# Kernel tuning notes

Hardware: AMD Instinct MI355X
Metric: run time of the kernel (lower is better)

## Reference

```python
import jax, jax.numpy as jnp
import numpy as np

H = 4096          # hidden_size
I = 11008         # intermediate_size
G = 128           # AWQ group_size
# AWQ interleaved nibble order within each packed int32
_ORDER = jnp.array([0, 4, 1, 5, 2, 6, 3, 7], dtype=jnp.int32) * 4


def _mk_lin(key, K, N):
    k1, k2, k3 = jax.random.split(key, 3)
    qw = jax.random.randint(k1, (K, N // 8), 0, 100, dtype=jnp.int32)
    qz = jax.random.randint(k2, (K // G, N // 8), 0, 100, dtype=jnp.int32)
    sc = jax.random.normal(k3, (K // G, N), dtype=jnp.float32) * 0.02
    return qw, qz, sc


def setup_inputs() -> dict:
    key = jax.random.key(0)
    ks = jax.random.split(key, 7)
    x = jax.random.normal(ks[0], (8, 16, H), dtype=jnp.float32)
    ln1_w = jnp.ones((H,), dtype=jnp.float32)
    ln2_w = jnp.ones((H,), dtype=jnp.float32)
    qkv_qw, qkv_qz, qkv_sc = _mk_lin(ks[1], H, 3 * H)
    o_qw, o_qz, o_sc = _mk_lin(ks[2], H, H)
    gu_qw, gu_qz, gu_sc = _mk_lin(ks[3], H, 2 * I)
    dn_qw, dn_qz, dn_sc = _mk_lin(ks[4], I, H)
    return dict(x=x, ln1_w=ln1_w, ln2_w=ln2_w,
                qkv_qw=qkv_qw, qkv_qz=qkv_qz, qkv_sc=qkv_sc,
                o_qw=o_qw, o_qz=o_qz, o_sc=o_sc,
                gu_qw=gu_qw, gu_qz=gu_qz, gu_sc=gu_sc,
                dn_qw=dn_qw, dn_qz=dn_qz, dn_sc=dn_sc)


def rmsnorm(x, w, eps=1e-6):
    return x * jax.lax.rsqrt(jnp.mean(x * x, axis=-1, keepdims=True) + eps) * w


def dequant(qw, qz, sc):
    # qw: [K, N//8] int32 -> [K, N]; qz: [K//G, N//8] -> [K//G, N]
    K = qw.shape[0]
    N = sc.shape[1]
    w = ((qw[:, :, None] >> _ORDER) & 0xF).reshape(K, N).astype(sc.dtype)
    z = ((qz[:, :, None] >> _ORDER) & 0xF).reshape(K // G, N).astype(sc.dtype)
    return (w - jnp.repeat(z, G, axis=0)) * jnp.repeat(sc, G, axis=0)


def lite_linear(x, qw, qz, sc):
    return x @ dequant(qw, qz, sc)


def reference(x, ln1_w, ln2_w,
              qkv_qw, qkv_qz, qkv_sc,
              o_qw, o_qz, o_sc,
              gu_qw, gu_qz, gu_sc,
              dn_qw, dn_qz, dn_sc):
    residual = x
    h = rmsnorm(x, ln1_w)
    h = lite_linear(h, qkv_qw, qkv_qz, qkv_sc)[..., :H]  # mock attn: take q slice
    h = lite_linear(h, o_qw, o_qz, o_sc)
    h = residual + h
    residual = h
    h = rmsnorm(h, ln2_w)
    gate_up = lite_linear(h, gu_qw, gu_qz, gu_sc)
    gate, up = gate_up[..., :I], gate_up[..., I:]
    h = lite_linear(jax.nn.silu(gate) * up, dn_qw, dn_qz, dn_sc)
    return residual + h
```

## Files before the change

kernel.cpp:

```cpp
#include <hip/hip_runtime.h>

typedef unsigned int   u32;
typedef unsigned short u16;

typedef __bf16 bf16x8 __attribute__((ext_vector_type(8)));
typedef float  f32x4  __attribute__((ext_vector_type(4)));

#define M_TOK 128

__device__ __forceinline__ u16 f2bf(float f) {
    u32 u = __builtin_bit_cast(u32, f);
    return (u16)((u + 0x8000u) >> 16);
}
__device__ __forceinline__ float bf2f(u16 h) {
    u32 u = ((u32)h) << 16;
    return __builtin_bit_cast(float, u);
}

__device__ __forceinline__ int rowoff(int r) { return r * 80 + (r >> 3) * 64; }

__launch_bounds__(256)
__global__ void rmsnorm_k(const float* __restrict__ in, const float* __restrict__ w,
                          u16* __restrict__ out) {
    const int row = blockIdx.x;
    const float* x = in + (size_t)row * 4096;
    float ss = 0.f;
#pragma unroll
    for (int j = 0; j < 16; ++j) {
        float v = x[threadIdx.x + 256 * j];
        ss += v * v;
    }
#pragma unroll
    for (int off = 32; off > 0; off >>= 1) ss += __shfl_down(ss, off, 64);
    __shared__ float ws4[4];
    if ((threadIdx.x & 63) == 0) ws4[threadIdx.x >> 6] = ss;
    __syncthreads();
    float total = ws4[0] + ws4[1] + ws4[2] + ws4[3];
    float r = rsqrtf(total * (1.f / 4096.f) + 1e-6f);
    u16* o = out + (size_t)row * 4096;
#pragma unroll
    for (int j = 0; j < 16; ++j) {
        int i = threadIdx.x + 256 * j;
        o[i] = f2bf(x[i] * r * w[i]);
    }
}

__launch_bounds__(256, 3)
__global__ void gemm_awq(const u16* __restrict__ A, const int* __restrict__ qw,
                         const int* __restrict__ qz, const float* __restrict__ sc,
                         u16* __restrict__ part,
                         int Astride, int qws, int scs, int N, int K, int kchunk) {
    __shared__ __align__(16) char ldsA[11264];
    __shared__ __align__(16) char ldsB[5632];

    const int tid = threadIdx.x;
    const int n0 = blockIdx.x * 64;
    const int sk = blockIdx.y;
    const int kc0 = sk * kchunk;
    const int kend = min(kc0 + kchunk, K);

    const int w    = tid >> 6;
    const int lane = tid & 63;
    const int wr  = (w >> 1) * 64;
    const int wc  = (w & 1) * 32;
    const int q   = lane >> 4;
    const int l16 = lane & 15;

    const int kp = tid & 15;
    const int p  = (tid >> 4) & 7;
    const int pc = (n0 >> 3) + p;
    const int nb = p * 704;

    const int ar = tid & 127;
    const u16* arow = A + (size_t)ar * Astride;
    char* adst = ldsA + rowoff(ar);

    f32x4 acc[4][2] = {};
    const u32 M4 = 0x0F0F0F0Fu;

    u32 zv = 0, w0c = 0, w1c = 0;
    float scv[8];
    uint4 a0c, a1c, a2c, a3c;
    if (tid < 128) {
        zv  = (u32)qz[(size_t)(kc0 >> 7) * qws + pc];
        const float* scp = sc + (size_t)(kc0 >> 7) * scs + n0 + p * 8;
        *(float4*)&scv[0] = *(const float4*)&scp[0];
        *(float4*)&scv[4] = *(const float4*)&scp[4];
        w0c = (u32)qw[(size_t)(kc0 + 2 * kp) * qws + pc];
        w1c = (u32)qw[(size_t)(kc0 + 2 * kp + 1) * qws + pc];
    } else {
        a0c = *(const uint4*)&arow[kc0 + 0];
        a1c = *(const uint4*)&arow[kc0 + 8];
        a2c = *(const uint4*)&arow[kc0 + 16];
        a3c = *(const uint4*)&arow[kc0 + 24];
    }

    for (int g0 = kc0; g0 < kend; g0 += 128) {
        const bool moreg = (g0 + 128) < kend;
        u32 zv_n = 0;
        float scv_n[8];
        u32 be = 0, bo = 0;
        if (tid < 128) {
            be = 0x10101010u - (zv & M4);
            bo = 0x10101010u - ((zv >> 4) & M4);
        }
#pragma unroll
        for (int s = 0; s < 4; ++s) {
            const int k0 = g0 + s * 32;
            const int kn = k0 + 32;
            if (tid < 128) {
                const u32 w0 = w0c, w1 = w1c;
                if (kn < kend) {
                    w0c = (u32)qw[(size_t)(kn + 2 * kp) * qws + pc];
                    w1c = (u32)qw[(size_t)(kn + 2 * kp + 1) * qws + pc];
                }
                if (s == 0 && moreg) {
                    zv_n = (u32)qz[(size_t)((g0 + 128) >> 7) * qws + pc];
                    const float* scp = sc + (size_t)((g0 + 128) >> 7) * scs + n0 + p * 8;
                    *(float4*)&scv_n[0] = *(const float4*)&scp[0];
                    *(float4*)&scv_n[4] = *(const float4*)&scp[4];
                }
                const u32 d0e = (w0 & M4) + be;
                const u32 d0o = ((w0 >> 4) & M4) + bo;
                const u32 d1e = (w1 & M4) + be;
                const u32 d1o = ((w1 >> 4) & M4) + bo;
                char* bbase = ldsB + nb + kp * 4;
                auto emit = [&](int j, u32 A0, u32 A1, int b) {
                    const float scj = scv[j];
                    const float off = -16.f * scj;
                    float f0 = fmaf((float)((A0 >> (8 * b)) & 0xFFu), scj, off);
                    float f1 = fmaf((float)((A1 >> (8 * b)) & 0xFFu), scj, off);
                    u32 u0 = __builtin_bit_cast(u32, f0) + 0x8000u;
                    u32 u1 = __builtin_bit_cast(u32, f1) + 0x8000u;
                    *(u32*)(bbase + j * 80) = __builtin_amdgcn_perm(u1, u0, 0x07060302u);
                };
                emit(0, d0e, d1e, 0); emit(4, d0e, d1e, 1);
                emit(1, d0e, d1e, 2); emit(5, d0e, d1e, 3);
                emit(2, d0o, d1o, 0); emit(6, d0o, d1o, 1);
                emit(3, d0o, d1o, 2); emit(7, d0o, d1o, 3);
            } else {
                const uint4 b0 = a0c, b1 = a1c, b2 = a2c, b3 = a3c;
                if (kn < kend) {
                    a0c = *(const uint4*)&arow[kn + 0];
                    a1c = *(const uint4*)&arow[kn + 8];
                    a2c = *(const uint4*)&arow[kn + 16];
                    a3c = *(const uint4*)&arow[kn + 24];
                }
                *(uint4*)(adst + 0)  = b0;
                *(uint4*)(adst + 16) = b1;
                *(uint4*)(adst + 32) = b2;
                *(uint4*)(adst + 48) = b3;
            }
            __syncthreads();

            bf16x8 af[4], bv[2];
#pragma unroll
            for (int mt = 0; mt < 4; ++mt)
                af[mt] = *(const bf16x8*)(ldsA + rowoff(wr + mt * 16 + l16) + q * 16);
#pragma unroll
            for (int nt = 0; nt < 2; ++nt)
                bv[nt] = *(const bf16x8*)(ldsB + rowoff(wc + nt * 16 + l16) + q * 16);
#pragma unroll
            for (int mt = 0; mt < 4; ++mt)
#pragma unroll
                for (int nt = 0; nt < 2; ++nt)
                    acc[mt][nt] = __builtin_amdgcn_mfma_f32_16x16x32_bf16(
                        af[mt], bv[nt], acc[mt][nt], 0, 0, 0);
            __syncthreads();
        }
        if (tid < 128 && moreg) {
            zv = zv_n;
#pragma unroll
            for (int j = 0; j < 8; ++j) scv[j] = scv_n[j];
        }
    }

    u16* pp = part + (size_t)sk * M_TOK * N;
#pragma unroll
    for (int mt = 0; mt < 4; ++mt) {
#pragma unroll
        for (int nt = 0; nt < 2; ++nt) {
            const int n = n0 + wc + nt * 16 + l16;
#pragma unroll
            for (int r = 0; r < 4; ++r) {
                const int m = wr + mt * 16 + q * 4 + r;
                pp[(size_t)m * N + n] = f2bf(acc[mt][nt][r]);
            }
        }
    }
}

__launch_bounds__(256)
__global__ void reduce_bf16(const u16* __restrict__ part, u16* __restrict__ out,
                            int total, int SK) {
    const int i = blockIdx.x * 256 + threadIdx.x;
    float s = 0.f;
    for (int k = 0; k < SK; ++k) s += bf2f(part[(size_t)k * total + i]);
    out[i] = f2bf(s);
}

__launch_bounds__(256)
__global__ void reduce_add_f32(const u16* __restrict__ part, const float* __restrict__ resin,
                               float* __restrict__ out, int total, int SK) {
    const int i = blockIdx.x * 256 + threadIdx.x;
    float s = resin[i];
    for (int k = 0; k < SK; ++k) s += bf2f(part[(size_t)k * total + i]);
    out[i] = s;
}

__launch_bounds__(256)
__global__ void silu_mul(const u16* __restrict__ part, u16* __restrict__ act) {
    const int n = blockIdx.x * 256 + threadIdx.x;
    const int m = blockIdx.y;
    const size_t plane = (size_t)M_TOK * 22016;
    const size_t base = (size_t)m * 22016;
    float g = bf2f(part[base + n]) + bf2f(part[plane + base + n]);
    float u = bf2f(part[base + n + 11008]) + bf2f(part[plane + base + n + 11008]);
    float a = g / (1.f + __expf(-g)) * u;
    act[(size_t)m * 11008 + n] = f2bf(a);
}

extern "C" void kernel_launch(void* const* d_in, const int* in_sizes, int n_in,
                              void* d_out, int out_size, void* d_ws, size_t ws_size,
                              hipStream_t stream) {
    const float* x      = (const float*)d_in[0];
    const float* ln1_w  = (const float*)d_in[1];
    const float* ln2_w  = (const float*)d_in[2];
    const int*   qkv_qw = (const int*)d_in[3];
    const int*   qkv_qz = (const int*)d_in[4];
    const float* qkv_sc = (const float*)d_in[5];
    const int*   o_qw   = (const int*)d_in[6];
    const int*   o_qz   = (const int*)d_in[7];
    const float* o_sc   = (const float*)d_in[8];
    const int*   gu_qw  = (const int*)d_in[9];
    const int*   gu_qz  = (const int*)d_in[10];
    const float* gu_sc  = (const float*)d_in[11];
    const int*   dn_qw  = (const int*)d_in[12];
    const int*   dn_qz  = (const int*)d_in[13];
    const float* dn_sc  = (const float*)d_in[14];
    float* out = (float*)d_out;

    char* ws = (char*)d_ws;
    u16*   pbuf = (u16*)(ws);
    u16*   slot = (u16*)(ws + 11534336);
    float* res2 = (float*)(ws + 12582912);
    u16*   act  = (u16*)(ws + 14680064);

    const int TOT = M_TOK * 4096;

    rmsnorm_k<<<128, 256, 0, stream>>>(x, ln1_w, slot);

    gemm_awq<<<dim3(64, 8), 256, 0, stream>>>(slot, qkv_qw, qkv_qz, qkv_sc, pbuf,
                                              4096, 1536, 12288, 4096, 4096, 512);
    reduce_bf16<<<2048, 256, 0, stream>>>(pbuf, slot, TOT, 8);

    gemm_awq<<<dim3(64, 8), 256, 0, stream>>>(slot, o_qw, o_qz, o_sc, pbuf,
                                              4096, 512, 4096, 4096, 4096, 512);
    reduce_add_f32<<<2048, 256, 0, stream>>>(pbuf, x, res2, TOT, 8);

    rmsnorm_k<<<128, 256, 0, stream>>>(res2, ln2_w, slot);

    gemm_awq<<<dim3(344, 2), 256, 0, stream>>>(slot, gu_qw, gu_qz, gu_sc, pbuf,
                                               4096, 2752, 22016, 22016, 4096, 2048);
    silu_mul<<<dim3(43, 128), 256, 0, stream>>>(pbuf, act);

    gemm_awq<<<dim3(64, 8), 256, 0, stream>>>(act, dn_qw, dn_qz, dn_sc, pbuf,
                                              11008, 512, 4096, 4096, 11008, 1408);
    reduce_add_f32<<<2048, 256, 0, stream>>>(pbuf, res2, out, TOT, 8);
}
```

Before: 338.9 us.

## Rewrite AWQ GEMM with fp16 magic-number dequant, double-buffered LDS and direct A loads

Switches activations, partials and the MFMA path from bf16 to fp16 and dequantizes nibbles with the 0x6400 magic-number trick in packed half math instead of per-element float FMAs. A is now loaded straight from global memory into registers rather than staged through LDS, B is double-buffered in LDS with 64-wide k steps, and weight loads are prefetched several steps ahead, leaving one barrier per step. Tiles are swizzled across blocks, and gate/up uses a 3-way k split with silu_mul summing three partials. The aim is less dequant ALU work and fewer sync stalls, at the cost of fp16 range and precision risk plus more register pressure.

```diff
diff --git a/kernel.cpp b/kernel.cpp
--- a/kernel.cpp
+++ b/kernel.cpp
@@ -3,21 +3,21 @@
 typedef unsigned int   u32;
 typedef unsigned short u16;
 
-typedef __bf16 bf16x8 __attribute__((ext_vector_type(8)));
-typedef float  f32x4  __attribute__((ext_vector_type(4)));
+typedef _Float16 h2  __attribute__((ext_vector_type(2)));
+typedef _Float16 h8  __attribute__((ext_vector_type(8)));
+typedef float    f32x4 __attribute__((ext_vector_type(4)));
 
 #define M_TOK 128
 
-__device__ __forceinline__ u16 f2bf(float f) {
-    u32 u = __builtin_bit_cast(u32, f);
-    return (u16)((u + 0x8000u) >> 16);
-}
-__device__ __forceinline__ float bf2f(u16 h) {
-    u32 u = ((u32)h) << 16;
-    return __builtin_bit_cast(float, u);
-}
-
-__device__ __forceinline__ int rowoff(int r) { return r * 80 + (r >> 3) * 64; }
+__device__ __forceinline__ void lds_barrier() {
+    asm volatile("s_waitcnt lgkmcnt(0)\n\ts_barrier" ::: "memory");
+}
+__device__ __forceinline__ u16 f2h_(float f) {
+    _Float16 h = (_Float16)f; return __builtin_bit_cast(u16, h);
+}
+__device__ __forceinline__ float h2f_(u16 b) {
+    _Float16 h = __builtin_bit_cast(_Float16, b); return (float)h;
+}
 
 __launch_bounds__(256)
 __global__ void rmsnorm_k(const float* __restrict__ in, const float* __restrict__ w,
@@ -41,7 +41,7 @@
 #pragma unroll
     for (int j = 0; j < 16; ++j) {
         int i = threadIdx.x + 256 * j;
-        o[i] = f2bf(x[i] * r * w[i]);
+        o[i] = f2h_(x[i] * r * w[i]);
     }
 }
 
@@ -50,153 +50,167 @@
                          const int* __restrict__ qz, const float* __restrict__ sc,
                          u16* __restrict__ part,
                          int Astride, int qws, int scs, int N, int K, int kchunk) {
-    __shared__ __align__(16) char ldsA[11264];
-    __shared__ __align__(16) char ldsB[5632];
+    __shared__ __align__(16) char ldsB[2 * 9216];
 
     const int tid = threadIdx.x;
-    const int n0 = blockIdx.x * 64;
+    int tile;
+    {
+        const int T = gridDim.x, bx = blockIdx.x, base = (T >> 4) << 4;
+        if (bx < base) { int a = bx >> 4, r = bx & 15; tile = a * 16 + ((r & 7) << 1) + (r >> 3); }
+        else tile = bx;
+    }
+    const int n0 = tile * 64;
     const int sk = blockIdx.y;
     const int kc0 = sk * kchunk;
     const int kend = min(kc0 + kchunk, K);
-
-    const int w    = tid >> 6;
-    const int lane = tid & 63;
-    const int wr  = (w >> 1) * 64;
-    const int wc  = (w & 1) * 32;
-    const int q   = lane >> 4;
-    const int l16 = lane & 15;
-
-    const int kp = tid & 15;
-    const int p  = (tid >> 4) & 7;
+    const int nsteps = (kend - kc0) >> 6;
+
+    const int w = tid >> 6, lane = tid & 63;
+    const int wr = (w >> 1) * 64, wc = (w & 1) * 32;
+    const int q = lane >> 4, l16 = lane & 15;
+
+    const int kp = tid & 31;
+    const int p = tid >> 5;
     const int pc = (n0 >> 3) + p;
-    const int nb = p * 704;
-
-    const int ar = tid & 127;
-    const u16* arow = A + (size_t)ar * Astride;
-    char* adst = ldsA + rowoff(ar);
+
+    const u16* ab[4];
+#pragma unroll
+    for (int mt = 0; mt < 4; ++mt)
+        ab[mt] = A + (size_t)(wr + mt * 16 + l16) * Astride + q * 8;
 
     f32x4 acc[4][2] = {};
-    const u32 M4 = 0x0F0F0F0Fu;
-
-    u32 zv = 0, w0c = 0, w1c = 0;
-    float scv[8];
-    uint4 a0c, a1c, a2c, a3c;
-    if (tid < 128) {
-        zv  = (u32)qz[(size_t)(kc0 >> 7) * qws + pc];
-        const float* scp = sc + (size_t)(kc0 >> 7) * scs + n0 + p * 8;
-        *(float4*)&scv[0] = *(const float4*)&scp[0];
-        *(float4*)&scv[4] = *(const float4*)&scp[4];
-        w0c = (u32)qw[(size_t)(kc0 + 2 * kp) * qws + pc];
-        w1c = (u32)qw[(size_t)(kc0 + 2 * kp + 1) * qws + pc];
-    } else {
-        a0c = *(const uint4*)&arow[kc0 + 0];
-        a1c = *(const uint4*)&arow[kc0 + 8];
-        a2c = *(const uint4*)&arow[kc0 + 16];
-        a3c = *(const uint4*)&arow[kc0 + 24];
-    }
-
-    for (int g0 = kc0; g0 < kend; g0 += 128) {
-        const bool moreg = (g0 + 128) < kend;
-        u32 zv_n = 0;
-        float scv_n[8];
-        u32 be = 0, bo = 0;
-        if (tid < 128) {
-            be = 0x10101010u - (zv & M4);
-            bo = 0x10101010u - ((zv >> 4) & M4);
-        }
-#pragma unroll
-        for (int s = 0; s < 4; ++s) {
-            const int k0 = g0 + s * 32;
-            const int kn = k0 + 32;
-            if (tid < 128) {
-                const u32 w0 = w0c, w1 = w1c;
-                if (kn < kend) {
-                    w0c = (u32)qw[(size_t)(kn + 2 * kp) * qws + pc];
-                    w1c = (u32)qw[(size_t)(kn + 2 * kp + 1) * qws + pc];
-                }
-                if (s == 0 && moreg) {
-                    zv_n = (u32)qz[(size_t)((g0 + 128) >> 7) * qws + pc];
-                    const float* scp = sc + (size_t)((g0 + 128) >> 7) * scs + n0 + p * 8;
-                    *(float4*)&scv_n[0] = *(const float4*)&scp[0];
-                    *(float4*)&scv_n[4] = *(const float4*)&scp[4];
-                }
-                const u32 d0e = (w0 & M4) + be;
-                const u32 d0o = ((w0 >> 4) & M4) + bo;
-                const u32 d1e = (w1 & M4) + be;
-                const u32 d1o = ((w1 >> 4) & M4) + bo;
-                char* bbase = ldsB + nb + kp * 4;
-                auto emit = [&](int j, u32 A0, u32 A1, int b) {
-                    const float scj = scv[j];
-                    const float off = -16.f * scj;
-                    float f0 = fmaf((float)((A0 >> (8 * b)) & 0xFFu), scj, off);
-                    float f1 = fmaf((float)((A1 >> (8 * b)) & 0xFFu), scj, off);
-                    u32 u0 = __builtin_bit_cast(u32, f0) + 0x8000u;
-                    u32 u1 = __builtin_bit_cast(u32, f1) + 0x8000u;
-                    *(u32*)(bbase + j * 80) = __builtin_amdgcn_perm(u1, u0, 0x07060302u);
-                };
-                emit(0, d0e, d1e, 0); emit(4, d0e, d1e, 1);
-                emit(1, d0e, d1e, 2); emit(5, d0e, d1e, 3);
-                emit(2, d0o, d1o, 0); emit(6, d0o, d1o, 1);
-                emit(3, d0o, d1o, 2); emit(7, d0o, d1o, 3);
-            } else {
-                const uint4 b0 = a0c, b1 = a1c, b2 = a2c, b3 = a3c;
-                if (kn < kend) {
-                    a0c = *(const uint4*)&arow[kn + 0];
-                    a1c = *(const uint4*)&arow[kn + 8];
-                    a2c = *(const uint4*)&arow[kn + 16];
-                    a3c = *(const uint4*)&arow[kn + 24];
-                }
-                *(uint4*)(adst + 0)  = b0;
-                *(uint4*)(adst + 16) = b1;
-                *(uint4*)(adst + 32) = b2;
-                *(uint4*)(adst + 48) = b3;
+    h2 mz[8], s2[8];
+    float rs[8];
+    u32 rawz = 0;
+    const int SH[8] = {0, 16, 4, 20, 8, 24, 12, 28};
+
+    auto ldqw = [&](int k, u32& a, u32& b) {
+        a = (u32)qw[(size_t)(k + 2 * kp) * qws + pc];
+        b = (u32)qw[(size_t)(k + 2 * kp + 1) * qws + pc];
+    };
+    auto lda = [&](int k, uint4(&dst)[8]) {
+#pragma unroll
+        for (int mt = 0; mt < 4; ++mt) {
+            dst[mt * 2 + 0] = *(const uint4*)(ab[mt] + k);
+            dst[mt * 2 + 1] = *(const uint4*)(ab[mt] + k + 32);
+        }
+    };
+    auto gconv = [&](u32 zword, const float* s8) {
+#pragma unroll
+        for (int j = 0; j < 8; ++j) {
+            u32 zj = (zword >> SH[j]) & 15u;
+            mz[j] = __builtin_bit_cast(h2, 0xE400E400u | zj | (zj << 16));
+            _Float16 hs = (_Float16)s8[j];
+            s2[j] = (h2){hs, hs};
+        }
+    };
+    auto deq = [&](u32 w0, u32 w1, char* wb) {
+        char* bb = wb + p * 1152 + kp * 4;
+        u32 w0s = w0 >> 4, w1s = w1 >> 4;
+        auto emit = [&](int j, u32 a0, u32 a1, int b) {
+            u32 t = __builtin_amdgcn_perm(a1, a0, (u32)(b | ((b + 4) << 16)));
+            u32 u = (t & 0x000F000Fu) | 0x64006400u;
+            h2 v = (__builtin_bit_cast(h2, u) + mz[j]) * s2[j];
+            *(u32*)(bb + j * 144) = __builtin_bit_cast(u32, v);
+        };
+        emit(0, w0, w1, 0);  emit(4, w0, w1, 1);
+        emit(1, w0, w1, 2);  emit(5, w0, w1, 3);
+        emit(2, w0s, w1s, 0); emit(6, w0s, w1s, 1);
+        emit(3, w0s, w1s, 2); emit(7, w0s, w1s, 3);
+    };
+    auto mm = [&](const uint4(&ac)[8], const char* rb) {
+        uint4 bf[4];
+#pragma unroll
+        for (int nt = 0; nt < 2; ++nt)
+#pragma unroll
+            for (int h = 0; h < 2; ++h)
+                bf[nt * 2 + h] = *(const uint4*)(rb + (wc + nt * 16 + l16) * 144 + h * 64 + q * 16);
+#pragma unroll
+        for (int mt = 0; mt < 4; ++mt)
+#pragma unroll
+            for (int nt = 0; nt < 2; ++nt)
+#pragma unroll
+                for (int h = 0; h < 2; ++h)
+                    acc[mt][nt] = __builtin_amdgcn_mfma_f32_16x16x32_f16(
+                        __builtin_bit_cast(h8, ac[mt * 2 + h]),
+                        __builtin_bit_cast(h8, bf[nt * 2 + h]),
+                        acc[mt][nt], 0, 0, 0);
+    };
+
+    const int g0 = kc0 >> 7;
+    u32 q0a, q0b, q1a, q1b, q2a, q2b;
+    uint4 aA[8], aB[8];
+    ldqw(kc0, q0a, q0b);
+    lda(kc0, aA);
+    ldqw(kc0 + 64, q1a, q1b);
+    ldqw(kc0 + 128, q2a, q2b);
+    {
+        u32 z0 = (u32)qz[(size_t)g0 * qws + pc];
+        const float* sp = sc + (size_t)g0 * scs + n0 + p * 8;
+        float t0[8];
+        *(float4*)&t0[0] = *(const float4*)sp;
+        *(float4*)&t0[4] = *(const float4*)(sp + 4);
+        gconv(z0, t0);
+    }
+    rawz = (u32)qz[(size_t)(g0 + 1) * qws + pc];
+    {
+        const float* sp = sc + (size_t)(g0 + 1) * scs + n0 + p * 8;
+        *(float4*)&rs[0] = *(const float4*)sp;
+        *(float4*)&rs[4] = *(const float4*)(sp + 4);
+    }
+    deq(q0a, q0b, ldsB);
+    lds_barrier();
+
+    auto body = [&](int s, uint4(&ac)[8], uint4(&an)[8], char* rb, char* wb, bool conv) {
+        const int kA = kc0 + ((s + 1) << 6);
+        const int kQ = kc0 + ((s + 3) << 6);
+        if (kA < kend) lda(kA, an);
+        u32 nqa = 0, nqb = 0;
+        if (kQ < kend) ldqw(kQ, nqa, nqb);
+        if (conv && kA < kend) {
+            float t0[8];
+#pragma unroll
+            for (int j = 0; j < 8; ++j) t0[j] = rs[j];
+            gconv(rawz, t0);
+            const int gn = (kA >> 7) + 1;
+            if ((gn << 7) < kend) {
+                rawz = (u32)qz[(size_t)gn * qws + pc];
+                const float* sp = sc + (size_t)gn * scs + n0 + p * 8;
+                *(float4*)&rs[0] = *(const float4*)sp;
+                *(float4*)&rs[4] = *(const float4*)(sp + 4);
             }
-            __syncthreads();
-
-            bf16x8 af[4], bv[2];
-#pragma unroll
-            for (int mt = 0; mt < 4; ++mt)
-                af[mt] = *(const bf16x8*)(ldsA + rowoff(wr + mt * 16 + l16) + q * 16);
-#pragma unroll
-            for (int nt = 0; nt < 2; ++nt)
-                bv[nt] = *(const bf16x8*)(ldsB + rowoff(wc + nt * 16 + l16) + q * 16);
-#pragma unroll
-            for (int mt = 0; mt < 4; ++mt)
-#pragma unroll
-                for (int nt = 0; nt < 2; ++nt)
-                    acc[mt][nt] = __builtin_amdgcn_mfma_f32_16x16x32_bf16(
-                        af[mt], bv[nt], acc[mt][nt], 0, 0, 0);
-            __syncthreads();
-        }
-        if (tid < 128 && moreg) {
-            zv = zv_n;
-#pragma unroll
-            for (int j = 0; j < 8; ++j) scv[j] = scv_n[j];
-        }
+        }
+        if (s + 1 < nsteps) deq(q1a, q1b, wb);
+        mm(ac, rb);
+        lds_barrier();
+        q1a = q2a; q1b = q2b; q2a = nqa; q2b = nqb;
+    };
+    for (int s = 0; s < nsteps; s += 2) {
+        body(s,     aA, aB, ldsB,        ldsB + 9216, false);
+        body(s + 1, aB, aA, ldsB + 9216, ldsB,        true);
     }
 
     u16* pp = part + (size_t)sk * M_TOK * N;
 #pragma unroll
-    for (int mt = 0; mt < 4; ++mt) {
+    for (int mt = 0; mt < 4; ++mt)
 #pragma unroll
         for (int nt = 0; nt < 2; ++nt) {
             const int n = n0 + wc + nt * 16 + l16;
 #pragma unroll
             for (int r = 0; r < 4; ++r) {
                 const int m = wr + mt * 16 + q * 4 + r;
-                pp[(size_t)m * N + n] = f2bf(acc[mt][nt][r]);
+                pp[(size_t)m * N + n] = f2h_(acc[mt][nt][r]);
             }
         }
-    }
-}
-
-__launch_bounds__(256)
-__global__ void reduce_bf16(const u16* __restrict__ part, u16* __restrict__ out,
-                            int total, int SK) {
+}
+
+__launch_bounds__(256)
+__global__ void reduce_f16(const u16* __restrict__ part, u16* __restrict__ out,
+                           int total, int SK) {
     const int i = blockIdx.x * 256 + threadIdx.x;
     float s = 0.f;
-    for (int k = 0; k < SK; ++k) s += bf2f(part[(size_t)k * total + i]);
-    out[i] = f2bf(s);
+    for (int k = 0; k < SK; ++k) s += h2f_(part[(size_t)k * total + i]);
+    out[i] = f2h_(s);
 }
 
 __launch_bounds__(256)
@@ -204,7 +218,7 @@
                                float* __restrict__ out, int total, int SK) {
     const int i = blockIdx.x * 256 + threadIdx.x;
     float s = resin[i];
-    for (int k = 0; k < SK; ++k) s += bf2f(part[(size_t)k * total + i]);
+    for (int k = 0; k < SK; ++k) s += h2f_(part[(size_t)k * total + i]);
     out[i] = s;
 }
 
@@ -214,10 +228,14 @@
     const int m = blockIdx.y;
     const size_t plane = (size_t)M_TOK * 22016;
     const size_t base = (size_t)m * 22016;
-    float g = bf2f(part[base + n]) + bf2f(part[plane + base + n]);
-    float u = bf2f(part[base + n + 11008]) + bf2f(part[plane + base + n + 11008]);
+    float g = 0.f, u = 0.f;
+#pragma unroll
+    for (int k = 0; k < 3; ++k) {
+        g += h2f_(part[(size_t)k * plane + base + n]);
+        u += h2f_(part[(size_t)k * plane + base + n + 11008]);
+    }
     float a = g / (1.f + __expf(-g)) * u;
-    act[(size_t)m * 11008 + n] = f2bf(a);
+    act[(size_t)m * 11008 + n] = f2h_(a);
 }
 
 extern "C" void kernel_launch(void* const* d_in, const int* in_sizes, int n_in,
@@ -242,9 +260,9 @@
 
     char* ws = (char*)d_ws;
     u16*   pbuf = (u16*)(ws);
-    u16*   slot = (u16*)(ws + 11534336);
-    float* res2 = (float*)(ws + 12582912);
-    u16*   act  = (u16*)(ws + 14680064);
+    u16*   act  = (u16*)(ws + 16908288);
+    float* res2 = (float*)(ws + 19726336);
+    u16*   slot = (u16*)(ws + 21823488);
 
     const int TOT = M_TOK * 4096;
 
@@ -252,7 +270,7 @@
 
     gemm_awq<<<dim3(64, 8), 256, 0, stream>>>(slot, qkv_qw, qkv_qz, qkv_sc, pbuf,
                                               4096, 1536, 12288, 4096, 4096, 512);
-    reduce_bf16<<<2048, 256, 0, stream>>>(pbuf, slot, TOT, 8);
+    reduce_f16<<<2048, 256, 0, stream>>>(pbuf, slot, TOT, 8);
 
     gemm_awq<<<dim3(64, 8), 256, 0, stream>>>(slot, o_qw, o_qz, o_sc, pbuf,
                                               4096, 512, 4096, 4096, 4096, 512);
@@ -260,8 +278,8 @@
 
     rmsnorm_k<<<128, 256, 0, stream>>>(res2, ln2_w, slot);
 
-    gemm_awq<<<dim3(344, 2), 256, 0, stream>>>(slot, gu_qw, gu_qz, gu_sc, pbuf,
-                                               4096, 2752, 22016, 22016, 4096, 2048);
+    gemm_awq<<<dim3(344, 3), 256, 0, stream>>>(slot, gu_qw, gu_qz, gu_sc, pbuf,
+                                               4096, 2752, 22016, 22016, 4096, 1408);
     silu_mul<<<dim3(43, 128), 256, 0, stream>>>(pbuf, act);
 
     gemm_awq<<<dim3(64, 8), 256, 0, stream>>>(act, dn_qw, dn_qz, dn_sc, pbuf,
```

New measurement: 407.2 us. +20.1%, slower.
